# Performance work log

Measured on AMD Instinct MI355X. Metric: run time of the kernel, lower is better.

The kernel has to match this reference:

```python
import jax, jax.numpy as jnp
import numpy as np

LAMBDA_CHAMFER = 1.0
LAMBDA_EDGE = 0.1


def setup_inputs() -> dict:
    key = jax.random.key(0)
    k1, k2, k3 = jax.random.split(key, 3)
    B, N, M, E = 8, 4096, 4096, 12288
    pred_vertices = jax.random.normal(k1, (B, N, 3), dtype=jnp.float32)
    gt_vertices = jax.random.normal(k2, (B, M, 3), dtype=jnp.float32)
    edges = jax.random.randint(k3, (E, 2), 0, N, dtype=jnp.int64)
    return {"pred_vertices": pred_vertices, "gt_vertices": gt_vertices, "edges": edges}


def _pairwise_dist(p1, p2):
    # ||x - y|| computed via the expanded form to avoid a [B,N,M,3] intermediate.
    # dist2[b,n,m] = |p1[b,n]|^2 + |p2[b,m]|^2 - 2 * p1[b,n] . p2[b,m]
    sq1 = jnp.sum(p1 * p1, axis=-1)  # [B, N]
    sq2 = jnp.sum(p2 * p2, axis=-1)  # [B, M]
    cross = jnp.einsum('bnd,bmd->bnm', p1, p2)  # [B, N, M]
    dist2 = sq1[:, :, None] + sq2[:, None, :] - 2.0 * cross
    return jnp.sqrt(jnp.maximum(dist2, 0.0))


def chamfer_distance(p1, p2):
    dist = _pairwise_dist(p1, p2)  # [B, N, M]
    min_p1 = jnp.min(dist, axis=2)  # [B, N] nearest gt for each pred point
    min_p2 = jnp.min(dist, axis=1)  # [B, M] nearest pred for each gt point
    return jnp.mean(min_p1) + jnp.mean(min_p2)


def edge_length_regularization(vertices, edges):
    v1 = vertices[:, edges[:, 0]]  # [B, E, 3]
    v2 = vertices[:, edges[:, 1]]  # [B, E, 3]
    lengths = jnp.linalg.norm(v1 - v2, axis=2)  # [B, E]
    return jnp.var(lengths, ddof=1)  # torch.var is unbiased by default


def reference(pred_vertices, gt_vertices, edges):
    cd = chamfer_distance(pred_vertices, gt_vertices)
    edge_loss = edge_length_regularization(pred_vertices, edges)
    return LAMBDA_CHAMFER * cd + LAMBDA_EDGE * edge_loss
```

## Files before the change

kernel.cpp:

```cpp
#include <hip/hip_runtime.h>
#include <hip/hip_bf16.h>
#include <float.h>

constexpr int B = 8, N = 4096, M = 4096, E = 12288;
constexpr int CBLOCK = 1024;
constexpr int EDGE_BLOCKS = (B * E) / CBLOCK;
constexpr int CHAM_BLOCKS = 2 * B * (N / 256);
constexpr int SPLIT = 64;
constexpr int RPT = M / SPLIT;
constexpr int VEC = 16;
constexpr int QB = 256;


__global__ __launch_bounds__(CBLOCK) void fused_kernel(
    const float* __restrict__ pred, const float* __restrict__ gt,
    const int* __restrict__ edges, float* __restrict__ ws) {
    const int bid = blockIdx.x;
    const int t = threadIdx.x;

    __shared__ float4 tile[M];
    __shared__ float wsum[16];
    float* red = (float*)tile;

    if (bid >= EDGE_BLOCKS) {
        const int cb  = bid - EDGE_BLOCKS;
        const int dir = cb >> 7;
        const int b   = (cb >> 4) & 7;
        const int qt  = cb & 15;
        const float* __restrict__ q   = dir ? gt   : pred;
        const float* __restrict__ ref = dir ? pred : gt;

        {
            const float2* rb = (const float2*)(ref + (size_t)b * M * 3) + 6 * t;
            const float2 r0 = rb[0], r1 = rb[1], r2 = rb[2];
            const float2 r3 = rb[3], r4 = rb[4], r5 = rb[5];
            const float x0=r0.x,y0=r0.y,z0=r1.x, x1=r1.y,y1=r2.x,z1=r2.y;
            const float x2=r3.x,y2=r3.y,z2=r4.x, x3=r4.y,y3=r5.x,z3=r5.y;
            tile[4*t+0] = make_float4(x0,y0,z0, 0.5f*(x0*x0+y0*y0+z0*z0));
            tile[4*t+1] = make_float4(x1,y1,z1, 0.5f*(x1*x1+y1*y1+z1*z1));
            tile[4*t+2] = make_float4(x2,y2,z2, 0.5f*(x2*x2+y2*y2+z2*z2));
            tile[4*t+3] = make_float4(x3,y3,z3, 0.5f*(x3*x3+y3*y3+z3*z3));
        }

        const int qloc = t & 15;
        const int s    = t >> 4;
        float qx[VEC], qy[VEC], qz[VEC];
#pragma unroll
        for (int i = 0; i < VEC; i++) {
            const int n = qt * QB + qloc + i * 16;
            const float* qp = q + ((size_t)b * N + n) * 3;
            qx[i] = qp[0]; qy[i] = qp[1]; qz[i] = qp[2];
        }
        __syncthreads();

        const float4* tl = tile + s * RPT;
        float mn[VEC];
#pragma unroll
        for (int i = 0; i < VEC; i++) mn[i] = FLT_MAX;

        float4 pA = tl[0], pB = tl[1];
#pragma unroll 2
        for (int m = 0; m < RPT - 2; m += 2) {
            const float4 nA = tl[m + 2], nB = tl[m + 3];
#pragma unroll
            for (int i = 0; i < VEC; i++) {
                float d0 = fmaf(-qz[i], pA.z, pA.w);
                d0 = fmaf(-qy[i], pA.y, d0);
                d0 = fmaf(-qx[i], pA.x, d0);
                float d1 = fmaf(-qz[i], pB.z, pB.w);
                d1 = fmaf(-qy[i], pB.y, d1);
                d1 = fmaf(-qx[i], pB.x, d1);
                mn[i] = fminf(mn[i], fminf(d0, d1));
            }
            pA = nA; pB = nB;
        }
#pragma unroll
        for (int i = 0; i < VEC; i++) {
            float d0 = fmaf(-qz[i], pA.z, pA.w);
            d0 = fmaf(-qy[i], pA.y, d0);
            d0 = fmaf(-qx[i], pA.x, d0);
            float d1 = fmaf(-qz[i], pB.z, pB.w);
            d1 = fmaf(-qy[i], pB.y, d1);
            d1 = fmaf(-qx[i], pB.x, d1);
            mn[i] = fminf(mn[i], fminf(d0, d1));
        }
        __syncthreads();

#pragma unroll
        for (int i = 0; i < VEC; i++)
            red[s * QB + qloc + i * 16] = mn[i];
        __syncthreads();

        float sv = 0.0f;
        if (t < QB) {
            float m = red[t];
#pragma unroll 8
            for (int k = 1; k < SPLIT; k++) m = fminf(m, red[k * QB + t]);
            const float* qp = q + ((size_t)b * N + qt * QB + t) * 3;
            const float sq = qp[0]*qp[0] + qp[1]*qp[1] + qp[2]*qp[2];
            sv = sqrtf(fmaxf(2.0f * m + sq, 0.0f));
        }
#pragma unroll
        for (int o = 32; o > 0; o >>= 1) sv += __shfl_down(sv, o, 64);
        if ((t & 63) == 0) wsum[t >> 6] = sv;
        __syncthreads();
        if (t == 0)
            ws[2 * EDGE_BLOCKS + cb] = wsum[0] + wsum[1] + wsum[2] + wsum[3];
    } else {
        const int eg = bid * CBLOCK + t;
        const int b  = eg / E;
        const int e  = eg - b * E;
        const int i0 = edges[2 * e], i1 = edges[2 * e + 1];
        const float* p0 = pred + ((size_t)b * N + i0) * 3;
        const float* p1 = pred + ((size_t)b * N + i1) * 3;
        const float dx = p0[0] - p1[0];
        const float dy = p0[1] - p1[1];
        const float dz = p0[2] - p1[2];
        float L  = sqrtf(dx * dx + dy * dy + dz * dz);
        float L2 = L * L;
#pragma unroll
        for (int o = 32; o > 0; o >>= 1) {
            L  += __shfl_down(L, o, 64);
            L2 += __shfl_down(L2, o, 64);
        }
        if ((t & 63) == 0) { red[t >> 6] = L; red[32 + (t >> 6)] = L2; }
        __syncthreads();
        if (t == 0) {
            float a = 0.0f, c = 0.0f;
#pragma unroll
            for (int w = 0; w < 16; w++) { a += red[w]; c += red[32 + w]; }
            ws[2 * bid]     = a;
            ws[2 * bid + 1] = c;
        }
    }
}

__global__ __launch_bounds__(256) void final_kernel(
    const float* __restrict__ ws, float* __restrict__ out) {
    const int t = threadIdx.x;
    float sc = ws[2 * EDGE_BLOCKS + t];
    float s1 = 0.0f, s2 = 0.0f;
    if (t < EDGE_BLOCKS) {
        s1 = ws[2 * t];
        s2 = ws[2 * t + 1];
    }
#pragma unroll
    for (int o = 32; o > 0; o >>= 1) {
        sc += __shfl_down(sc, o, 64);
        s1 += __shfl_down(s1, o, 64);
        s2 += __shfl_down(s2, o, 64);
    }
    __shared__ float w[3][4];
    const int wv = t >> 6, ln = t & 63;
    if (ln == 0) { w[0][wv] = sc; w[1][wv] = s1; w[2][wv] = s2; }
    __syncthreads();
    if (t == 0) {
        float S = 0.0f, A = 0.0f, C = 0.0f;
#pragma unroll
        for (int i = 0; i < 4; i++) { S += w[0][i]; A += w[1][i]; C += w[2][i]; }
        const float K = (float)(B * E);
        const float var = (C - A * A / K) / (K - 1.0f);
        out[0] = S / 32768.0f + 0.1f * var;
    }
}

extern "C" void kernel_launch(void* const* d_in, const int* in_sizes, int n_in,
                              void* d_out, int out_size, void* d_ws, size_t ws_size,
                              hipStream_t stream) {
    const float* pred  = (const float*)d_in[0];
    const float* gt    = (const float*)d_in[1];
    const int*   edges = (const int*)d_in[2];
    float* out = (float*)d_out;
    float* wsf = (float*)d_ws;

    fused_kernel<<<EDGE_BLOCKS + CHAM_BLOCKS, CBLOCK, 0, stream>>>(pred, gt, edges, wsf);
    final_kernel<<<1, 256, 0, stream>>>(wsf, out);
}
```

Baseline: 83.92 us.

## Prepack points into float4 workspace and stream reference points from global memory

```diff
diff --git a/kernel.cpp b/kernel.cpp
--- a/kernel.cpp
+++ b/kernel.cpp
@@ -3,65 +3,63 @@
 #include <float.h>
 
 constexpr int B = 8, N = 4096, M = 4096, E = 12288;
-constexpr int CBLOCK = 1024;
-constexpr int EDGE_BLOCKS = (B * E) / CBLOCK;
-constexpr int CHAM_BLOCKS = 2 * B * (N / 256);
-constexpr int SPLIT = 64;
+constexpr int TB = 512;
+constexpr int EDGE_BLOCKS = (B * E) / TB;
+constexpr int QB = 128;
+constexpr int CHAM_BLOCKS = 2 * B * (N / QB);
+constexpr int SPLIT = 32;
 constexpr int RPT = M / SPLIT;
-constexpr int VEC = 16;
-constexpr int QB = 256;
+constexpr int VEC = 8;
+constexpr int NPTS = 2 * B * N;
 
 
-__global__ __launch_bounds__(CBLOCK) void fused_kernel(
+__global__ __launch_bounds__(256) void pack_kernel(
     const float* __restrict__ pred, const float* __restrict__ gt,
-    const int* __restrict__ edges, float* __restrict__ ws) {
+    float4* __restrict__ pts4) {
+    const int i = blockIdx.x * 256 + threadIdx.x;
+    const float* src = (i < B * N) ? pred : gt;
+    const float* p = src + (size_t)(i & (B * N - 1)) * 3;
+    const float x = p[0], y = p[1], z = p[2];
+    pts4[i] = make_float4(x, y, z, 0.5f * (x * x + y * y + z * z));
+}
+
+__global__ __launch_bounds__(TB) void fused_kernel(
+    const float* __restrict__ pred, const int* __restrict__ edges,
+    const float4* __restrict__ pts4, float* __restrict__ wsf) {
     const int bid = blockIdx.x;
     const int t = threadIdx.x;
 
-    __shared__ float4 tile[M];
-    __shared__ float wsum[16];
-    float* red = (float*)tile;
+    __shared__ float red[SPLIT * QB];
+    __shared__ float wsum[8], wsum2[8];
 
     if (bid >= EDGE_BLOCKS) {
         const int cb  = bid - EDGE_BLOCKS;
-        const int dir = cb >> 7;
-        const int b   = (cb >> 4) & 7;
-        const int qt  = cb & 15;
-        const float* __restrict__ q   = dir ? gt   : pred;
-        const float* __restrict__ ref = dir ? pred : gt;
+        const int dir = cb >> 8;
+        const int b   = (cb >> 5) & 7;
+        const int qt  = cb & 31;
+        const float4* __restrict__ q4 = pts4 + (dir ? B * N : 0) + b * N;
+        const float4* __restrict__ r4 = pts4 + (dir ? 0 : B * N) + b * M;
 
-        {
-            const float2* rb = (const float2*)(ref + (size_t)b * M * 3) + 6 * t;
-            const float2 r0 = rb[0], r1 = rb[1], r2 = rb[2];
-            const float2 r3 = rb[3], r4 = rb[4], r5 = rb[5];
-            const float x0=r0.x,y0=r0.y,z0=r1.x, x1=r1.y,y1=r2.x,z1=r2.y;
-            const float x2=r3.x,y2=r3.y,z2=r4.x, x3=r4.y,y3=r5.x,z3=r5.y;
-            tile[4*t+0] = make_float4(x0,y0,z0, 0.5f*(x0*x0+y0*y0+z0*z0));
-            tile[4*t+1] = make_float4(x1,y1,z1, 0.5f*(x1*x1+y1*y1+z1*z1));
-            tile[4*t+2] = make_float4(x2,y2,z2, 0.5f*(x2*x2+y2*y2+z2*z2));
-            tile[4*t+3] = make_float4(x3,y3,z3, 0.5f*(x3*x3+y3*y3+z3*z3));
-        }
+        const int ql = t & 15;
+        const int s  = t >> 4;
 
-        const int qloc = t & 15;
-        const int s    = t >> 4;
         float qx[VEC], qy[VEC], qz[VEC];
 #pragma unroll
         for (int i = 0; i < VEC; i++) {
-            const int n = qt * QB + qloc + i * 16;
-            const float* qp = q + ((size_t)b * N + n) * 3;
-            qx[i] = qp[0]; qy[i] = qp[1]; qz[i] = qp[2];
+            const float4 Q = q4[qt * QB + ql + i * 16];
+            qx[i] = Q.x; qy[i] = Q.y; qz[i] = Q.z;
         }
-        __syncthreads();
 
-        const float4* tl = tile + s * RPT;
+        const float4* __restrict__ tb = r4 + s * RPT;
         float mn[VEC];
 #pragma unroll
         for (int i = 0; i < VEC; i++) mn[i] = FLT_MAX;
 
-        float4 pA = tl[0], pB = tl[1];
+        float4 pA = tb[0], pB = tb[1], pC = tb[2], pD = tb[3];
 #pragma unroll 2
-        for (int m = 0; m < RPT - 2; m += 2) {
-            const float4 nA = tl[m + 2], nB = tl[m + 3];
+        for (int m = 0; m < RPT - 4; m += 4) {
+            const float4 nA = tb[m + 4], nB = tb[m + 5];
+            const float4 nC = tb[m + 6], nD = tb[m + 7];
 #pragma unroll
             for (int i = 0; i < VEC; i++) {
                 float d0 = fmaf(-qz[i], pA.z, pA.w);
@@ -70,9 +68,16 @@
                 float d1 = fmaf(-qz[i], pB.z, pB.w);
                 d1 = fmaf(-qy[i], pB.y, d1);
                 d1 = fmaf(-qx[i], pB.x, d1);
+                float d2 = fmaf(-qz[i], pC.z, pC.w);
+                d2 = fmaf(-qy[i], pC.y, d2);
+                d2 = fmaf(-qx[i], pC.x, d2);
+                float d3 = fmaf(-qz[i], pD.z, pD.w);
+                d3 = fmaf(-qy[i], pD.y, d3);
+                d3 = fmaf(-qx[i], pD.x, d3);
                 mn[i] = fminf(mn[i], fminf(d0, d1));
+                mn[i] = fminf(mn[i], fminf(d2, d3));
             }
-            pA = nA; pB = nB;
+            pA = nA; pB = nB; pC = nC; pD = nD;
         }
 #pragma unroll
         for (int i = 0; i < VEC; i++) {
@@ -82,13 +87,19 @@
             float d1 = fmaf(-qz[i], pB.z, pB.w);
             d1 = fmaf(-qy[i], pB.y, d1);
             d1 = fmaf(-qx[i], pB.x, d1);
+            float d2 = fmaf(-qz[i], pC.z, pC.w);
+            d2 = fmaf(-qy[i], pC.y, d2);
+            d2 = fmaf(-qx[i], pC.x, d2);
+            float d3 = fmaf(-qz[i], pD.z, pD.w);
+            d3 = fmaf(-qy[i], pD.y, d3);
+            d3 = fmaf(-qx[i], pD.x, d3);
             mn[i] = fminf(mn[i], fminf(d0, d1));
+            mn[i] = fminf(mn[i], fminf(d2, d3));
         }
-        __syncthreads();
 
 #pragma unroll
         for (int i = 0; i < VEC; i++)
-            red[s * QB + qloc + i * 16] = mn[i];
+            red[s * QB + ql + i * 16] = mn[i];
         __syncthreads();
 
         float sv = 0.0f;
@@ -96,18 +107,17 @@
             float m = red[t];
 #pragma unroll 8
             for (int k = 1; k < SPLIT; k++) m = fminf(m, red[k * QB + t]);
-            const float* qp = q + ((size_t)b * N + qt * QB + t) * 3;
-            const float sq = qp[0]*qp[0] + qp[1]*qp[1] + qp[2]*qp[2];
-            sv = sqrtf(fmaxf(2.0f * m + sq, 0.0f));
+            const float4 Q = q4[qt * QB + t];
+            sv = sqrtf(fmaxf(2.0f * m + (Q.w + Q.w), 0.0f));
         }
 #pragma unroll
         for (int o = 32; o > 0; o >>= 1) sv += __shfl_down(sv, o, 64);
         if ((t & 63) == 0) wsum[t >> 6] = sv;
         __syncthreads();
         if (t == 0)
-            ws[2 * EDGE_BLOCKS + cb] = wsum[0] + wsum[1] + wsum[2] + wsum[3];
+            wsf[2 * EDGE_BLOCKS + cb] = wsum[0] + wsum[1];
     } else {
-        const int eg = bid * CBLOCK + t;
+        const int eg = bid * TB + t;
         const int b  = eg / E;
         const int e  = eg - b * E;
         const int i0 = edges[2 * e], i1 = edges[2 * e + 1];
@@ -123,26 +133,27 @@
             L  += __shfl_down(L, o, 64);
             L2 += __shfl_down(L2, o, 64);
         }
-        if ((t & 63) == 0) { red[t >> 6] = L; red[32 + (t >> 6)] = L2; }
+        const int wv = t >> 6;
+        if ((t & 63) == 0) { wsum[wv] = L; wsum2[wv] = L2; }
         __syncthreads();
         if (t == 0) {
             float a = 0.0f, c = 0.0f;
 #pragma unroll
-            for (int w = 0; w < 16; w++) { a += red[w]; c += red[32 + w]; }
-            ws[2 * bid]     = a;
-            ws[2 * bid + 1] = c;
+            for (int w = 0; w < 8; w++) { a += wsum[w]; c += wsum2[w]; }
+            wsf[2 * bid]     = a;
+            wsf[2 * bid + 1] = c;
         }
     }
 }
 
-__global__ __launch_bounds__(256) void final_kernel(
-    const float* __restrict__ ws, float* __restrict__ out) {
+__global__ __launch_bounds__(TB) void final_kernel(
+    const float* __restrict__ wsf, float* __restrict__ out) {
     const int t = threadIdx.x;
-    float sc = ws[2 * EDGE_BLOCKS + t];
+    float sc = wsf[2 * EDGE_BLOCKS + t];
     float s1 = 0.0f, s2 = 0.0f;
     if (t < EDGE_BLOCKS) {
-        s1 = ws[2 * t];
-        s2 = ws[2 * t + 1];
+        s1 = wsf[2 * t];
+        s2 = wsf[2 * t + 1];
     }
 #pragma unroll
     for (int o = 32; o > 0; o >>= 1) {
@@ -150,14 +161,14 @@
         s1 += __shfl_down(s1, o, 64);
         s2 += __shfl_down(s2, o, 64);
     }
-    __shared__ float w[3][4];
+    __shared__ float w[3][8];
     const int wv = t >> 6, ln = t & 63;
     if (ln == 0) { w[0][wv] = sc; w[1][wv] = s1; w[2][wv] = s2; }
     __syncthreads();
     if (t == 0) {
         float S = 0.0f, A = 0.0f, C = 0.0f;
 #pragma unroll
-        for (int i = 0; i < 4; i++) { S += w[0][i]; A += w[1][i]; C += w[2][i]; }
+        for (int i = 0; i < 8; i++) { S += w[0][i]; A += w[1][i]; C += w[2][i]; }
         const float K = (float)(B * E);
         const float var = (C - A * A / K) / (K - 1.0f);
         out[0] = S / 32768.0f + 0.1f * var;
@@ -171,8 +182,10 @@
     const float* gt    = (const float*)d_in[1];
     const int*   edges = (const int*)d_in[2];
     float* out = (float*)d_out;
-    float* wsf = (float*)d_ws;
+    float4* pts4 = (float4*)d_ws;
+    float*  wsf  = (float*)d_ws + (size_t)4 * NPTS;
 
-    fused_kernel<<<EDGE_BLOCKS + CHAM_BLOCKS, CBLOCK, 0, stream>>>(pred, gt, edges, wsf);
-    final_kernel<<<1, 256, 0, stream>>>(wsf, out);
+    pack_kernel<<<NPTS / 256, 256, 0, stream>>>(pred, gt, pts4);
+    fused_kernel<<<EDGE_BLOCKS + CHAM_BLOCKS, TB, 0, stream>>>(pred, edges, pts4, wsf);
+    final_kernel<<<1, TB, 0, stream>>>(wsf, out);
 }
```

Result: slower. 85.96 us (+2.4%).
